# Optimization experiments

Measured on AMD Instinct MI355X. Metric: run time of the kernel, lower is better.

Reference implementation:

```python
import jax, jax.numpy as jnp
import numpy as np


def setup_inputs() -> dict:
    key = jax.random.key(0)
    k1, k2, k3, k4 = jax.random.split(key, 4)
    B, T, C = 4, 2048, 1024
    x = jax.random.normal(k1, (B, T, C), dtype=jnp.float32)
    scale = 1.0 / np.sqrt(C)
    Wq = jax.random.normal(k2, (C, C), dtype=jnp.float32) * scale
    Wk = jax.random.normal(k3, (C, C), dtype=jnp.float32) * scale
    Wv = jax.random.normal(k4, (C, C), dtype=jnp.float32) * scale
    return {"x": x, "Wq": Wq, "Wk": Wk, "Wv": Wv}


def reference(x, Wq, Wk, Wv):
    # x: [B, T, C]; torch Linear(no bias): y = x @ W.T
    B, T, C = x.shape
    q = jnp.einsum('btc,dc->btd', x, Wq)
    k = jnp.einsum('btc,dc->btd', x, Wk)
    v = jnp.einsum('btc,dc->btd', x, Wv)
    scale = jnp.asarray(C, x.dtype) ** -0.5
    qk = jnp.einsum('bqd,bkd->bqk', q, k) * scale  # [B, T, T]
    causal = jnp.tril(jnp.ones((T, T), dtype=bool))
    qk = jnp.where(causal, qk, -jnp.inf)
    attn = jax.nn.softmax(qk, axis=-1)
    out = jnp.einsum('bqk,bkd->bqd', attn, v)
    return out
```

## Files before the change

kernel.cpp:

```cpp
#include <hip/hip_runtime.h>

typedef __attribute__((ext_vector_type(8))) short  short8;
typedef __attribute__((ext_vector_type(4))) short  short4v;
typedef __attribute__((ext_vector_type(4))) float  floatx4;

__device__ inline short f2bf(float f) {
    union { float f; unsigned u; } v; v.f = f;
    unsigned r = v.u + 0x7fffu + ((v.u >> 16) & 1u);
    return (short)(r >> 16);
}

typedef const __attribute__((address_space(1))) unsigned int* gp1_t;
typedef __attribute__((address_space(3))) unsigned int* lp3_t;

__device__ __attribute__((always_inline)) inline void gl_lds16(const short* g, short* l) {
    __builtin_amdgcn_global_load_lds((gp1_t)g, (lp3_t)l, 16, 0, 0);
}

__device__ __attribute__((always_inline)) inline void gemm_bt_core(
    const short* __restrict__ Ag, const short* __restrict__ Bg,
    int lda, int ldb, int kmax,
    short* As, short* Bs, floatx4 acc[4][4])
{
    const int t    = threadIdx.x;
    const int srow = t >> 3;
    const int scol = (t & 7) * 8;
    const int lane = t & 63;
    const int wid  = t >> 6;
    const int wx   = wid & 1, wy = wid >> 1;
    const int lm   = lane & 15, lq = lane >> 4;

    for (int k0 = 0; k0 < kmax; k0 += 64) {
        __syncthreads();
#pragma unroll
        for (int i = 0; i < 4; ++i) {
            gl_lds16(Ag + (size_t)(i * 32 + srow) * lda + k0 + scol,
                     As + (i * 32 + srow) * 64 + scol);
            gl_lds16(Bg + (size_t)(i * 32 + srow) * ldb + k0 + scol,
                     Bs + (i * 32 + srow) * 64 + scol);
        }
        __syncthreads();

#pragma unroll
        for (int ks = 0; ks < 2; ++ks) {
            short8 af[4], bfr[4];
#pragma unroll
            for (int mi = 0; mi < 4; ++mi)
                af[mi] = *(const short8*)(As + (wy * 64 + mi * 16 + lm) * 64 + ks * 32 + lq * 8);
#pragma unroll
            for (int ni = 0; ni < 4; ++ni)
                bfr[ni] = *(const short8*)(Bs + (wx * 64 + ni * 16 + lm) * 64 + ks * 32 + lq * 8);
#pragma unroll
            for (int mi = 0; mi < 4; ++mi)
#pragma unroll
                for (int ni = 0; ni < 4; ++ni)
                    acc[mi][ni] = __builtin_amdgcn_mfma_f32_16x16x32_bf16(
                        af[mi], bfr[ni], acc[mi][ni], 0, 0, 0);
        }
    }
}

__global__ void cast_all(const float* __restrict__ x,
                         const float* __restrict__ Wq,
                         const float* __restrict__ Wk,
                         const float* __restrict__ Wv,
                         short* __restrict__ xb, short* __restrict__ wb,
                         float* __restrict__ lsum)
{
    size_t v = (size_t)blockIdx.x * 256 + threadIdx.x;
    const float* src; short* dst; size_t off;
    if (v < 2097152)      { src = x;  dst = xb;           off = v; }
    else if (v < 2359296) { src = Wq; dst = wb;           off = v - 2097152; }
    else if (v < 2621440) { src = Wk; dst = wb + 1048576; off = v - 2359296; }
    else if (v < 2883584) { src = Wv; dst = wb + 2097152; off = v - 2621440; }
    else if (v < 2885632) {
        floatx4 z = {0.f, 0.f, 0.f, 0.f};
        ((floatx4*)lsum)[v - 2883584] = z;
        return;
    } else return;
    floatx4 vv = ((const floatx4*)src)[off];
    short4v s;
#pragma unroll
    for (int e = 0; e < 4; ++e) s[e] = f2bf(vv[e]);
    ((short4v*)dst)[off] = s;
}

__global__ __launch_bounds__(256, 3) void qkv_gemm(
    const short* __restrict__ xb, const short* __restrict__ wb,
    short* __restrict__ qb, short* __restrict__ kb, short* __restrict__ vt)
{
    __shared__ short As[128 * 64];
    __shared__ short Bs[128 * 64];

    const int m0    = blockIdx.x * 128;
    const int which = blockIdx.y >> 3;
    const int n0    = (blockIdx.y & 7) * 128;

    floatx4 acc[4][4];
    floatx4 zero = {0.f, 0.f, 0.f, 0.f};
#pragma unroll
    for (int i = 0; i < 4; ++i)
#pragma unroll
        for (int j = 0; j < 4; ++j) acc[i][j] = zero;

    gemm_bt_core(xb + (size_t)m0 * 1024,
                 wb + (size_t)blockIdx.y * 128 * 1024,
                 1024, 1024, 1024, As, Bs, acc);

    const int lane = threadIdx.x & 63, wid = threadIdx.x >> 6;
    const int wx = wid & 1, wy = wid >> 1, lm = lane & 15, lq = lane >> 4;
#pragma unroll
    for (int mi = 0; mi < 4; ++mi)
#pragma unroll
        for (int ni = 0; ni < 4; ++ni)
#pragma unroll
            for (int r = 0; r < 4; ++r) {
                int row = m0 + wy * 64 + mi * 16 + lq * 4 + r;
                int col = n0 + wx * 64 + ni * 16 + lm;
                short bvv = f2bf(acc[mi][ni][r]);
                if (which == 2) {
                    int bb = row >> 11, tt = row & 2047;
                    vt[((size_t)bb * 1024 + col) * 2048 + tt] = bvv;
                } else if (which == 1) {
                    kb[(size_t)row * 1024 + col] = bvv;
                } else {
                    qb[(size_t)row * 1024 + col] = bvv;
                }
            }
}

__global__ __launch_bounds__(256, 3) void sqk_gemm(
    const short* __restrict__ qb, const short* __restrict__ kb,
    short* __restrict__ P, float* __restrict__ lsum)
{
    int idx = blockIdx.x;
    int i = 0;
    while ((i + 1) * (i + 2) / 2 <= idx) ++i;
    const int j = idx - i * (i + 1) / 2;
    const int b = blockIdx.y;

    __shared__ short As[128 * 64];
    __shared__ short Bs[128 * 64];

    floatx4 acc[4][4];
    floatx4 zero = {0.f, 0.f, 0.f, 0.f};
#pragma unroll
    for (int a = 0; a < 4; ++a)
#pragma unroll
        for (int c = 0; c < 4; ++c) acc[a][c] = zero;

    gemm_bt_core(qb + ((size_t)(b * 2048 + i * 128)) * 1024,
                 kb + ((size_t)(b * 2048 + j * 128)) * 1024,
                 1024, 1024, 1024, As, Bs, acc);

    const float sscl = 0.03125f * 1.44269504089f;
    const bool  diag = (i == j);
    const int lane = threadIdx.x & 63, wid = threadIdx.x >> 6;
    const int wx = wid & 1, wy = wid >> 1, lm = lane & 15, lq = lane >> 4;

#pragma unroll
    for (int mi = 0; mi < 4; ++mi)
#pragma unroll
        for (int r = 0; r < 4; ++r) {
            const int lrow = wy * 64 + mi * 16 + lq * 4 + r;
            const int grow = i * 128 + lrow;
            short* prow = P + ((size_t)b * 2048 + grow) * 2048 + j * 128;
            float rsum = 0.f;
#pragma unroll
            for (int ni = 0; ni < 4; ++ni) {
                const int lcol = wx * 64 + ni * 16 + lm;
                float p = exp2f(acc[mi][ni][r] * sscl);
                if (diag && lcol > lrow) p = 0.f;
                rsum += p;
                prow[lcol] = f2bf(p);
            }
#pragma unroll
            for (int off = 1; off < 16; off <<= 1) rsum += __shfl_xor(rsum, off);
            if (lm == 0) atomicAdd(lsum + b * 2048 + grow, rsum);
        }
}

__global__ __launch_bounds__(256, 3) void pv_gemm(
    const short* __restrict__ P, const short* __restrict__ vt,
    const float* __restrict__ lsum, float* __restrict__ out)
{
    const int x  = blockIdx.x;
    const int pr = blockIdx.y;
    const int b  = blockIdx.z;
    const int n0 = x * 64;

    __shared__ short As[128 * 64];
    __shared__ short Bs[64 * 64];

    const int t    = threadIdx.x;
    const int srow = t >> 3;
    const int scol = (t & 7) * 8;
    const int lane = t & 63;
    const int wid  = t >> 6;
    const int wx   = wid & 1, wy = wid >> 1;
    const int lm   = lane & 15, lq = lane >> 4;

    const short* Bg = vt + ((size_t)b * 1024 + n0) * 2048;

#pragma unroll
    for (int phase = 0; phase < 2; ++phase) {
        const int i    = phase ? (15 - pr) : pr;
        const int kmax = (i + 1) * 128;
        const short* Ag = P + ((size_t)b * 2048 + i * 128) * 2048;

        floatx4 acc[4][2];
        floatx4 zero = {0.f, 0.f, 0.f, 0.f};
#pragma unroll
        for (int a = 0; a < 4; ++a)
#pragma unroll
            for (int c = 0; c < 2; ++c) acc[a][c] = zero;

        for (int k0 = 0; k0 < kmax; k0 += 64) {
            __syncthreads();
#pragma unroll
            for (int q = 0; q < 4; ++q)
                gl_lds16(Ag + (size_t)(q * 32 + srow) * 2048 + k0 + scol,
                         As + (q * 32 + srow) * 64 + scol);
#pragma unroll
            for (int q = 0; q < 2; ++q)
                gl_lds16(Bg + (size_t)(q * 32 + srow) * 2048 + k0 + scol,
                         Bs + (q * 32 + srow) * 64 + scol);
            __syncthreads();

#pragma unroll
            for (int ks = 0; ks < 2; ++ks) {
                short8 af[4], bfr[2];
#pragma unroll
                for (int mi = 0; mi < 4; ++mi)
                    af[mi] = *(const short8*)(As + (wy * 64 + mi * 16 + lm) * 64 + ks * 32 + lq * 8);
#pragma unroll
                for (int ni = 0; ni < 2; ++ni)
                    bfr[ni] = *(const short8*)(Bs + (wx * 32 + ni * 16 + lm) * 64 + ks * 32 + lq * 8);
#pragma unroll
                for (int mi = 0; mi < 4; ++mi)
#pragma unroll
                    for (int ni = 0; ni < 2; ++ni)
                        acc[mi][ni] = __builtin_amdgcn_mfma_f32_16x16x32_bf16(
                            af[mi], bfr[ni], acc[mi][ni], 0, 0, 0);
            }
        }

#pragma unroll
        for (int mi = 0; mi < 4; ++mi)
#pragma unroll
            for (int r = 0; r < 4; ++r) {
                const int grow = b * 2048 + i * 128 + wy * 64 + mi * 16 + lq * 4 + r;
                const float li = 1.0f / lsum[grow];
#pragma unroll
                for (int ni = 0; ni < 2; ++ni)
                    out[(size_t)grow * 1024 + n0 + wx * 32 + ni * 16 + lm] =
                        acc[mi][ni][r] * li;
            }
    }
}

extern "C" void kernel_launch(void* const* d_in, const int* in_sizes, int n_in,
                              void* d_out, int out_size, void* d_ws, size_t ws_size,
                              hipStream_t stream)
{
    (void)in_sizes; (void)n_in; (void)out_size; (void)ws_size;
    const float* x  = (const float*)d_in[0];
    const float* Wq = (const float*)d_in[1];
    const float* Wk = (const float*)d_in[2];
    const float* Wv = (const float*)d_in[3];
    float* out = (float*)d_out;

    char* base = (char*)d_ws;
    short* xb   = (short*)(base);
    short* wb   = (short*)(base + 16777216);
    short* qb   = (short*)(base + 23068672);
    short* kb   = (short*)(base + 39845888);
    short* vt   = (short*)(base + 56623104);
    short* P    = (short*)(base + 73400320);
    float* lsum = (float*)(base + 107954176);

    cast_all<<<11272, 256, 0, stream>>>(x, Wq, Wk, Wv, xb, wb, lsum);
    qkv_gemm<<<dim3(64, 24), 256, 0, stream>>>(xb, wb, qb, kb, vt);
    sqk_gemm<<<dim3(136, 4), 256, 0, stream>>>(qb, kb, P, lsum);
    pv_gemm<<<dim3(16, 8, 4), 256, 0, stream>>>(P, vt, lsum, out);
}
```

Before: 245.8 us.

## Compute softmax row sums in PV GEMM via ones-vector MFMA, drop atomics

Removes the shuffle reduction and atomicAdd of row sums from the score kernel. The denominator is instead computed inside the PV GEMM as an extra MFMA against a vector of bf16 ones, so it sums the same rounded P values that feed the GEMM. PV is retiled to 128x128 blocks with one row-block per workgroup, replacing the previous pairing of short and long causal rows, and the GEMM launch bounds are raised to 4 waves. The extra MFMA column adds roughly a quarter more matrix work in PV, and the new grid is imbalanced across rows because of causal lengths.

```diff
diff --git a/kernel.cpp b/kernel.cpp
--- a/kernel.cpp
+++ b/kernel.cpp
@@ -64,8 +64,7 @@
                          const float* __restrict__ Wq,
                          const float* __restrict__ Wk,
                          const float* __restrict__ Wv,
-                         short* __restrict__ xb, short* __restrict__ wb,
-                         float* __restrict__ lsum)
+                         short* __restrict__ xb, short* __restrict__ wb)
 {
     size_t v = (size_t)blockIdx.x * 256 + threadIdx.x;
     const float* src; short* dst; size_t off;
@@ -73,11 +72,7 @@
     else if (v < 2359296) { src = Wq; dst = wb;           off = v - 2097152; }
     else if (v < 2621440) { src = Wk; dst = wb + 1048576; off = v - 2359296; }
     else if (v < 2883584) { src = Wv; dst = wb + 2097152; off = v - 2621440; }
-    else if (v < 2885632) {
-        floatx4 z = {0.f, 0.f, 0.f, 0.f};
-        ((floatx4*)lsum)[v - 2883584] = z;
-        return;
-    } else return;
+    else return;
     floatx4 vv = ((const floatx4*)src)[off];
     short4v s;
 #pragma unroll
@@ -85,7 +80,7 @@
     ((short4v*)dst)[off] = s;
 }
 
-__global__ __launch_bounds__(256, 3) void qkv_gemm(
+__global__ __launch_bounds__(256, 4) void qkv_gemm(
     const short* __restrict__ xb, const short* __restrict__ wb,
     short* __restrict__ qb, short* __restrict__ kb, short* __restrict__ vt)
 {
@@ -129,9 +124,9 @@
             }
 }
 
-__global__ __launch_bounds__(256, 3) void sqk_gemm(
+__global__ __launch_bounds__(256, 4) void sqk_gemm(
     const short* __restrict__ qb, const short* __restrict__ kb,
-    short* __restrict__ P, float* __restrict__ lsum)
+    short* __restrict__ P)
 {
     int idx = blockIdx.x;
     int i = 0;
@@ -165,32 +160,26 @@
             const int lrow = wy * 64 + mi * 16 + lq * 4 + r;
             const int grow = i * 128 + lrow;
             short* prow = P + ((size_t)b * 2048 + grow) * 2048 + j * 128;
-            float rsum = 0.f;
 #pragma unroll
             for (int ni = 0; ni < 4; ++ni) {
                 const int lcol = wx * 64 + ni * 16 + lm;
                 float p = exp2f(acc[mi][ni][r] * sscl);
                 if (diag && lcol > lrow) p = 0.f;
-                rsum += p;
                 prow[lcol] = f2bf(p);
             }
-#pragma unroll
-            for (int off = 1; off < 16; off <<= 1) rsum += __shfl_xor(rsum, off);
-            if (lm == 0) atomicAdd(lsum + b * 2048 + grow, rsum);
         }
 }
 
 __global__ __launch_bounds__(256, 3) void pv_gemm(
     const short* __restrict__ P, const short* __restrict__ vt,
-    const float* __restrict__ lsum, float* __restrict__ out)
-{
-    const int x  = blockIdx.x;
-    const int pr = blockIdx.y;
-    const int b  = blockIdx.z;
-    const int n0 = x * 64;
+    float* __restrict__ out)
+{
+    const int x = blockIdx.x, i = blockIdx.y, b = blockIdx.z;
+    const int n0 = x * 128;
+    const int kmax = (i + 1) * 128;
 
     __shared__ short As[128 * 64];
-    __shared__ short Bs[64 * 64];
+    __shared__ short Bs[128 * 64];
 
     const int t    = threadIdx.x;
     const int srow = t >> 3;
@@ -200,63 +189,63 @@
     const int wx   = wid & 1, wy = wid >> 1;
     const int lm   = lane & 15, lq = lane >> 4;
 
+    const short* Ag = P  + ((size_t)b * 2048 + i * 128) * 2048;
     const short* Bg = vt + ((size_t)b * 1024 + n0) * 2048;
 
-#pragma unroll
-    for (int phase = 0; phase < 2; ++phase) {
-        const int i    = phase ? (15 - pr) : pr;
-        const int kmax = (i + 1) * 128;
-        const short* Ag = P + ((size_t)b * 2048 + i * 128) * 2048;
-
-        floatx4 acc[4][2];
-        floatx4 zero = {0.f, 0.f, 0.f, 0.f};
-#pragma unroll
-        for (int a = 0; a < 4; ++a)
-#pragma unroll
-            for (int c = 0; c < 2; ++c) acc[a][c] = zero;
-
-        for (int k0 = 0; k0 < kmax; k0 += 64) {
-            __syncthreads();
-#pragma unroll
-            for (int q = 0; q < 4; ++q)
-                gl_lds16(Ag + (size_t)(q * 32 + srow) * 2048 + k0 + scol,
-                         As + (q * 32 + srow) * 64 + scol);
-#pragma unroll
-            for (int q = 0; q < 2; ++q)
-                gl_lds16(Bg + (size_t)(q * 32 + srow) * 2048 + k0 + scol,
-                         Bs + (q * 32 + srow) * 64 + scol);
-            __syncthreads();
-
-#pragma unroll
-            for (int ks = 0; ks < 2; ++ks) {
-                short8 af[4], bfr[2];
-#pragma unroll
-                for (int mi = 0; mi < 4; ++mi)
-                    af[mi] = *(const short8*)(As + (wy * 64 + mi * 16 + lm) * 64 + ks * 32 + lq * 8);
-#pragma unroll
-                for (int ni = 0; ni < 2; ++ni)
-                    bfr[ni] = *(const short8*)(Bs + (wx * 32 + ni * 16 + lm) * 64 + ks * 32 + lq * 8);
-#pragma unroll
-                for (int mi = 0; mi < 4; ++mi)
-#pragma unroll
-                    for (int ni = 0; ni < 2; ++ni)
-                        acc[mi][ni] = __builtin_amdgcn_mfma_f32_16x16x32_bf16(
-                            af[mi], bfr[ni], acc[mi][ni], 0, 0, 0);
+    floatx4 acc[4][5];
+    floatx4 zero = {0.f, 0.f, 0.f, 0.f};
+#pragma unroll
+    for (int a = 0; a < 4; ++a)
+#pragma unroll
+        for (int c = 0; c < 5; ++c) acc[a][c] = zero;
+
+    short8 vones;
+#pragma unroll
+    for (int e = 0; e < 8; ++e) vones[e] = (short)0x3F80;
+
+    for (int k0 = 0; k0 < kmax; k0 += 64) {
+        __syncthreads();
+#pragma unroll
+        for (int q = 0; q < 4; ++q) {
+            gl_lds16(Ag + (size_t)(q * 32 + srow) * 2048 + k0 + scol,
+                     As + (q * 32 + srow) * 64 + scol);
+            gl_lds16(Bg + (size_t)(q * 32 + srow) * 2048 + k0 + scol,
+                     Bs + (q * 32 + srow) * 64 + scol);
+        }
+        __syncthreads();
+
+#pragma unroll
+        for (int ks = 0; ks < 2; ++ks) {
+            short8 af[4], bfr[4];
+#pragma unroll
+            for (int mi = 0; mi < 4; ++mi)
+                af[mi] = *(const short8*)(As + (wy * 64 + mi * 16 + lm) * 64 + ks * 32 + lq * 8);
+#pragma unroll
+            for (int ni = 0; ni < 4; ++ni)
+                bfr[ni] = *(const short8*)(Bs + (wx * 64 + ni * 16 + lm) * 64 + ks * 32 + lq * 8);
+#pragma unroll
+            for (int mi = 0; mi < 4; ++mi) {
+#pragma unroll
+                for (int ni = 0; ni < 4; ++ni)
+                    acc[mi][ni] = __builtin_amdgcn_mfma_f32_16x16x32_bf16(
+                        af[mi], bfr[ni], acc[mi][ni], 0, 0, 0);
+                acc[mi][4] = __builtin_amdgcn_mfma_f32_16x16x32_bf16(
+                    af[mi], vones, acc[mi][4], 0, 0, 0);
             }
         }
-
-#pragma unroll
-        for (int mi = 0; mi < 4; ++mi)
-#pragma unroll
-            for (int r = 0; r < 4; ++r) {
-                const int grow = b * 2048 + i * 128 + wy * 64 + mi * 16 + lq * 4 + r;
-                const float li = 1.0f / lsum[grow];
-#pragma unroll
-                for (int ni = 0; ni < 2; ++ni)
-                    out[(size_t)grow * 1024 + n0 + wx * 32 + ni * 16 + lm] =
-                        acc[mi][ni][r] * li;
-            }
     }
+
+#pragma unroll
+    for (int mi = 0; mi < 4; ++mi)
+#pragma unroll
+        for (int r = 0; r < 4; ++r) {
+            const int grow = b * 2048 + i * 128 + wy * 64 + mi * 16 + lq * 4 + r;
+            const float li = 1.0f / acc[mi][4][r];
+#pragma unroll
+            for (int ni = 0; ni < 4; ++ni)
+                out[(size_t)grow * 1024 + n0 + wx * 64 + ni * 16 + lm] =
+                    acc[mi][ni][r] * li;
+        }
 }
 
 extern "C" void kernel_launch(void* const* d_in, const int* in_sizes, int n_in,
@@ -271,16 +260,15 @@
     float* out = (float*)d_out;
 
     char* base = (char*)d_ws;
-    short* xb   = (short*)(base);
-    short* wb   = (short*)(base + 16777216);
-    short* qb   = (short*)(base + 23068672);
-    short* kb   = (short*)(base + 39845888);
-    short* vt   = (short*)(base + 56623104);
-    short* P    = (short*)(base + 73400320);
-    float* lsum = (float*)(base + 107954176);
-
-    cast_all<<<11272, 256, 0, stream>>>(x, Wq, Wk, Wv, xb, wb, lsum);
+    short* xb = (short*)(base);
+    short* wb = (short*)(base + 16777216);
+    short* qb = (short*)(base + 23068672);
+    short* kb = (short*)(base + 39845888);
+    short* vt = (short*)(base + 56623104);
+    short* P  = (short*)(base + 73400320);
+
+    cast_all<<<11264, 256, 0, stream>>>(x, Wq, Wk, Wv, xb, wb);
     qkv_gemm<<<dim3(64, 24), 256, 0, stream>>>(xb, wb, qb, kb, vt);
-    sqk_gemm<<<dim3(136, 4), 256, 0, stream>>>(qb, kb, P, lsum);
-    pv_gemm<<<dim3(16, 8, 4), 256, 0, stream>>>(P, vt, lsum, out);
-}
+    sqk_gemm<<<dim3(136, 4), 256, 0, stream>>>(qb, kb, P);
+    pv_gemm<<<dim3(8, 16, 4), 256, 0, stream>>>(P, vt, out);
+}
```

Result: slower. 251.2 us (+2.2%).
